# Optimization experiments

Hardware: AMD Instinct MI355X
Metric: run time of the kernel (lower is better)

Reference implementation:

```python
import jax, jax.numpy as jnp
import numpy as np

B, S, H = 64, 2048, 512


def _xavier(key, shape):
    fan_in, fan_out = shape[-1], shape[-2] if len(shape) > 1 else 1
    limit = float(np.sqrt(6.0 / (fan_in + fan_out)))
    return jax.random.uniform(key, shape, jnp.float32, -limit, limit)


def setup_inputs() -> dict:
    key = jax.random.key(0)
    k1, k2, k3, k4, k5, k6 = jax.random.split(key, 6)
    keys_ = jax.random.normal(k1, (B, S, H), jnp.float32)
    query = jax.random.normal(k2, (B, H), jnp.float32)
    v1 = _xavier(k3, (H,))
    W1 = _xavier(k4, (H, 2 * H))
    v2 = _xavier(k5, (H,))
    W2 = _xavier(k6, (H, 2 * H))
    return {"keys": keys_, "query": query, "v1": v1, "W1": W1, "v2": v2, "W2": W2}


def reference(keys, query, v1, W1, v2, W2):
    b, s, h = keys.shape
    # Stage 1: additive (Bahdanau) scoring over concat(keys, broadcast query)
    q = jnp.broadcast_to(query[:, None, :], (b, s, h))          # [B,S,H]
    hidden = jnp.concatenate([keys, q], axis=2)                  # [B,S,2H]
    t1 = jnp.tanh(jnp.einsum('de,bse->bsd', W1, hidden))         # [B,S,H]
    scores = jnp.einsum('d,bsd->bs', v1, t1)                     # [B,S]
    attns = jax.nn.softmax(scores, axis=1)                       # [B,S]
    # values == keys in the original module
    new_q = jnp.einsum('bs,bsh->bh', attns, keys)                # [B,H]
    # Stage 2: score again against concat(keys, broadcast new_query)
    nq = jnp.broadcast_to(new_q[:, None, :], (b, s, h))
    hidden2 = jnp.concatenate([keys, nq], axis=2)                # [B,S,2H]
    t2 = jnp.tanh(jnp.einsum('de,bse->bsd', W2, hidden2))        # [B,S,H]
    attn_vecs = jnp.einsum('d,bsd->bs', v2, t2)[:, None, :]      # [B,1,S]
    return attn_vecs
```

## Files before the change

kernel.cpp:

```cpp
#include <hip/hip_runtime.h>
#include <cstdint>
#include <cstddef>

#define S_DIM 2048

typedef __attribute__((ext_vector_type(8))) short short8;
typedef __attribute__((ext_vector_type(4))) float f32x4;

static __device__ __forceinline__ unsigned short f2bf(float f) {
  union { float f; unsigned int u; } v; v.f = f;
  unsigned int r = (v.u + 0x7fffu + ((v.u >> 16) & 1u)) >> 16;
  return (unsigned short)r;
}

static __device__ __forceinline__ float bf2f(unsigned short u) {
  union { unsigned int u; float f; } v; v.u = ((unsigned int)u) << 16;
  return v.f;
}

static __device__ __forceinline__ float fast_tanh(float x) {
  x = fminf(15.f, fmaxf(-15.f, x));
  float e = __expf(x + x);
  return 1.f - 2.f * __builtin_amdgcn_rcpf(e + 1.f);
}

static __device__ __forceinline__ void gload_lds16(const void* g, void* l) {
  __builtin_amdgcn_global_load_lds(
      (const __attribute__((address_space(1))) void*)g,
      (__attribute__((address_space(3))) void*)l, 16, 0, 0);
}


__global__ __launch_bounds__(256) void pack_b_kernel(
    const float* __restrict__ W1, const float* __restrict__ W2,
    unsigned short* __restrict__ wkp1, unsigned short* __restrict__ wkp2) {
  int j = blockIdx.x * 256 + threadIdx.x;
  const float* W = (j < 32768) ? W1 : W2;
  unsigned short* o = (j < 32768) ? wkp1 : wkp2;
  int wt = j & 32767;
  int k0 = wt >> 11, g = (wt >> 6) & 31, lhi = (wt >> 4) & 3, l15 = wt & 15;
  const float* src = W + (size_t)(g * 16 + l15) * 1024 + k0 * 32 + lhi * 8;
  float4 f0 = *reinterpret_cast<const float4*>(src);
  float4 f1 = *reinterpret_cast<const float4*>(src + 4);
  short8 hv;
  hv[0] = (short)f2bf(f0.x); hv[1] = (short)f2bf(f0.y);
  hv[2] = (short)f2bf(f0.z); hv[3] = (short)f2bf(f0.w);
  hv[4] = (short)f2bf(f1.x); hv[5] = (short)f2bf(f1.y);
  hv[6] = (short)f2bf(f1.z); hv[7] = (short)f2bf(f1.w);
  *reinterpret_cast<short8*>(o + (size_t)wt * 8) = hv;
}

__global__ __launch_bounds__(512, 2) void fused_pack_scores_kernel(
    const float* __restrict__ keys, const unsigned short* __restrict__ wkp,
    const float* __restrict__ v, const float* __restrict__ qp,
    unsigned short* __restrict__ akp, float* __restrict__ scores1) {
  __shared__ __align__(16) unsigned short lds_a[32768];
  __shared__ float lds_score[8][64];

  const int tid  = threadIdx.x;
  const int wid  = tid >> 6;
  const int lane = tid & 63;
  const int l15  = lane & 15;
  const int lhi  = lane >> 4;
  const int tile = blockIdx.x;
  const int row0 = tile * 64;
  const int b    = row0 >> 11;
  const int wcol = wid * 64;

  {
    const int s_mr  = (tid >> 6) & 3;
    const int s_lhi = (tid >> 4) & 3;
    const int s_l15 = tid & 15;
    const int k0_0  = tid >> 8;
    const float* srow =
        keys + (size_t)(row0 + s_mr * 16 + s_l15) * 512 + s_lhi * 8;
    unsigned short* atile = akp + (size_t)tile * 32768;
    float4 f[8][2];
    #pragma unroll
    for (int i = 0; i < 8; ++i) {
      const int k0 = k0_0 + 2 * i;
      const float* src = srow + k0 * 32;
      f[i][0] = *reinterpret_cast<const float4*>(src);
      f[i][1] = *reinterpret_cast<const float4*>(src + 4);
    }
    __builtin_amdgcn_sched_barrier(0);
    #pragma unroll
    for (int i = 0; i < 8; ++i) {
      const int c = i * 512 + tid;
      short8 hv;
      hv[0] = (short)f2bf(f[i][0].x); hv[1] = (short)f2bf(f[i][0].y);
      hv[2] = (short)f2bf(f[i][0].z); hv[3] = (short)f2bf(f[i][0].w);
      hv[4] = (short)f2bf(f[i][1].x); hv[5] = (short)f2bf(f[i][1].y);
      hv[6] = (short)f2bf(f[i][1].z); hv[7] = (short)f2bf(f[i][1].w);
      *reinterpret_cast<short8*>((char*)lds_a + c * 16) = hv;
      *reinterpret_cast<short8*>(atile + (size_t)c * 8) = hv;
    }
  }

  const unsigned short* wbase = wkp + (size_t)wid * 2048 + (size_t)lane * 8;
  short8 bb[2][4];
  #pragma unroll
  for (int nc = 0; nc < 4; ++nc)
    bb[0][nc] = *reinterpret_cast<const short8*>(wbase + nc * 512);

  __syncthreads();

  f32x4 acc[4][4];
  #pragma unroll
  for (int mr = 0; mr < 4; ++mr)
    #pragma unroll
    for (int nc = 0; nc < 4; ++nc) {
      f32x4 z = {0.f, 0.f, 0.f, 0.f};
      acc[mr][nc] = z;
    }

  const char* abase = (const char*)lds_a + lane * 16;

  #pragma unroll
  for (int k0 = 0; k0 < 16; ++k0) {
    const int cur = k0 & 1, nxt = cur ^ 1;
    if (k0 < 15) {
      #pragma unroll
      for (int nc = 0; nc < 4; ++nc)
        bb[nxt][nc] = *reinterpret_cast<const short8*>(
            wbase + (size_t)(k0 + 1) * 16384 + nc * 512);
    }
    short8 a[4];
    #pragma unroll
    for (int mr = 0; mr < 4; ++mr)
      a[mr] = *reinterpret_cast<const short8*>(abase + k0 * 4096 + mr * 1024);
    #pragma unroll
    for (int mr = 0; mr < 4; ++mr)
      #pragma unroll
      for (int nc = 0; nc < 4; ++nc)
        acc[mr][nc] = __builtin_amdgcn_mfma_f32_16x16x32_bf16(
            a[mr], bb[cur][nc], acc[mr][nc], 0, 0, 0);
  }

  float rp[4][4];
  #pragma unroll
  for (int mr = 0; mr < 4; ++mr)
    #pragma unroll
    for (int j = 0; j < 4; ++j) rp[mr][j] = 0.f;

  #pragma unroll
  for (int nc = 0; nc < 4; ++nc) {
    int col = wcol + nc * 16 + l15;
    float vv = v[col];
    float qv = qp[b * 512 + col];
    #pragma unroll
    for (int mr = 0; mr < 4; ++mr)
      #pragma unroll
      for (int j = 0; j < 4; ++j)
        rp[mr][j] += fast_tanh(acc[mr][nc][j] + qv) * vv;
  }

  #pragma unroll
  for (int off = 1; off < 16; off <<= 1)
    #pragma unroll
    for (int mr = 0; mr < 4; ++mr)
      #pragma unroll
      for (int j = 0; j < 4; ++j)
        rp[mr][j] += __shfl_xor(rp[mr][j], off, 64);

  if (l15 == 0) {
    #pragma unroll
    for (int mr = 0; mr < 4; ++mr)
      #pragma unroll
      for (int j = 0; j < 4; ++j)
        lds_score[wid][mr * 16 + lhi * 4 + j] = rp[mr][j];
  }
  __syncthreads();
  if (tid < 64) {
    float s = 0.f;
    #pragma unroll
    for (int w = 0; w < 8; ++w) s += lds_score[w][tid];
    scores1[row0 + tid] = s;
  }
}

__global__ __launch_bounds__(512, 4) void fused_packed_kernel(
    const unsigned short* __restrict__ akp, const unsigned short* __restrict__ wkp,
    const float* __restrict__ v, const float* __restrict__ qp,
    float* __restrict__ out) {
  __shared__ __align__(16) unsigned short lds_a[32768];
  __shared__ float lds_score[8][64];

  const int tid  = threadIdx.x;
  const int wid  = tid >> 6;
  const int lane = tid & 63;
  const int l15  = lane & 15;
  const int lhi  = lane >> 4;
  const int tile = blockIdx.x;
  const int row0 = tile * 64;
  const int b    = row0 >> 11;
  const int wcol = wid * 64;

  const unsigned short* atile = akp + (size_t)tile * 32768;
  #pragma unroll
  for (int i = 0; i < 8; ++i)
    gload_lds16(atile + (i * 512 + tid) * 8, (char*)lds_a + (i * 512 + tid) * 16);

  const unsigned short* wbase = wkp + (size_t)wid * 2048 + (size_t)lane * 8;
  short8 bb[2][4];
  #pragma unroll
  for (int nc = 0; nc < 4; ++nc)
    bb[0][nc] = *reinterpret_cast<const short8*>(wbase + nc * 512);

  __syncthreads();

  f32x4 acc[4][4];
  #pragma unroll
  for (int mr = 0; mr < 4; ++mr)
    #pragma unroll
    for (int nc = 0; nc < 4; ++nc) {
      f32x4 z = {0.f, 0.f, 0.f, 0.f};
      acc[mr][nc] = z;
    }

  const char* abase = (const char*)lds_a + lane * 16;

  #pragma unroll
  for (int k0 = 0; k0 < 16; ++k0) {
    const int cur = k0 & 1, nxt = cur ^ 1;
    if (k0 < 15) {
      #pragma unroll
      for (int nc = 0; nc < 4; ++nc)
        bb[nxt][nc] = *reinterpret_cast<const short8*>(
            wbase + (size_t)(k0 + 1) * 16384 + nc * 512);
    }
    short8 a[4];
    #pragma unroll
    for (int mr = 0; mr < 4; ++mr)
      a[mr] = *reinterpret_cast<const short8*>(abase + k0 * 4096 + mr * 1024);
    #pragma unroll
    for (int mr = 0; mr < 4; ++mr)
      #pragma unroll
      for (int nc = 0; nc < 4; ++nc)
        acc[mr][nc] = __builtin_amdgcn_mfma_f32_16x16x32_bf16(
            a[mr], bb[cur][nc], acc[mr][nc], 0, 0, 0);
  }

  float rp[4][4];
  #pragma unroll
  for (int mr = 0; mr < 4; ++mr)
    #pragma unroll
    for (int j = 0; j < 4; ++j) rp[mr][j] = 0.f;

  #pragma unroll
  for (int nc = 0; nc < 4; ++nc) {
    int col = wcol + nc * 16 + l15;
    float vv = v[col];
    float qv = qp[b * 512 + col];
    #pragma unroll
    for (int mr = 0; mr < 4; ++mr)
      #pragma unroll
      for (int j = 0; j < 4; ++j)
        rp[mr][j] += fast_tanh(acc[mr][nc][j] + qv) * vv;
  }

  #pragma unroll
  for (int off = 1; off < 16; off <<= 1)
    #pragma unroll
    for (int mr = 0; mr < 4; ++mr)
      #pragma unroll
      for (int j = 0; j < 4; ++j)
        rp[mr][j] += __shfl_xor(rp[mr][j], off, 64);

  if (l15 == 0) {
    #pragma unroll
    for (int mr = 0; mr < 4; ++mr)
      #pragma unroll
      for (int j = 0; j < 4; ++j)
        lds_score[wid][mr * 16 + lhi * 4 + j] = rp[mr][j];
  }
  __syncthreads();
  if (tid < 64) {
    float s = 0.f;
    #pragma unroll
    for (int w = 0; w < 8; ++w) s += lds_score[w][tid];
    out[row0 + tid] = s;
  }
}

__global__ __launch_bounds__(256) void wsum_packed_kernel(
    const unsigned short* __restrict__ akp, const float* __restrict__ attn,
    float* __restrict__ new_q) {
  int b = blockIdx.x, k0 = blockIdx.y;
  int t = threadIdx.x;
  int mr = t >> 6, lhi = (t >> 4) & 3, l15 = t & 15;
  const unsigned short* base =
      akp + (size_t)b * 32 * 32768 + (size_t)k0 * 2048 + (size_t)t * 8;
  const float* ab = attn + b * S_DIM + mr * 16 + l15;
  float acc[8];
  #pragma unroll
  for (int e = 0; e < 8; ++e) acc[e] = 0.f;
  #pragma unroll 4
  for (int tile = 0; tile < 32; ++tile) {
    short8 kv = *reinterpret_cast<const short8*>(base + (size_t)tile * 32768);
    float w = ab[tile * 64];
    #pragma unroll
    for (int e = 0; e < 8; ++e)
      acc[e] += w * bf2f((unsigned short)kv[e]);
  }
  __shared__ float red[4][64][8];
  #pragma unroll
  for (int e = 0; e < 8; ++e) red[lhi][mr * 16 + l15][e] = acc[e];
  __syncthreads();
  if (t < 32) {
    int lh = t >> 3, e = t & 7;
    float s = 0.f;
    #pragma unroll 8
    for (int r = 0; r < 64; ++r) s += red[lh][r][e];
    new_q[b * 512 + k0 * 32 + lh * 8 + e] = s;
  }
}


__global__ __launch_bounds__(512) void qproj_kernel(
    const float* __restrict__ W, const float* __restrict__ x,
    float* __restrict__ qp) {
  __shared__ float xs[512];
  int b = blockIdx.x, d = threadIdx.x;
  xs[d] = x[b * 512 + d];
  __syncthreads();
  const float4* wr = (const float4*)(W + (size_t)d * 1024 + 512);
  const float4* xv = (const float4*)xs;
  float acc = 0.f;
  #pragma unroll 8
  for (int h = 0; h < 128; ++h) {
    float4 w4 = wr[h], x4 = xv[h];
    acc += w4.x * x4.x + w4.y * x4.y + w4.z * x4.z + w4.w * x4.w;
  }
  qp[b * 512 + d] = acc;
}

__global__ __launch_bounds__(256) void softmax_kernel(float* __restrict__ sc) {
  int b = blockIdx.x, tid = threadIdx.x;
  float* row = sc + (size_t)b * S_DIM;
  float vv[8];
  float m = -1e30f;
  #pragma unroll
  for (int i = 0; i < 8; ++i) { vv[i] = row[tid + i * 256]; m = fmaxf(m, vv[i]); }
  #pragma unroll
  for (int off = 32; off; off >>= 1) m = fmaxf(m, __shfl_xor(m, off, 64));
  __shared__ float red[4], red2[4];
  int wid = tid >> 6, lane = tid & 63;
  if (lane == 0) red[wid] = m;
  __syncthreads();
  m = fmaxf(fmaxf(red[0], red[1]), fmaxf(red[2], red[3]));
  float s = 0.f;
  #pragma unroll
  for (int i = 0; i < 8; ++i) { vv[i] = __expf(vv[i] - m); s += vv[i]; }
  #pragma unroll
  for (int off = 32; off; off >>= 1) s += __shfl_xor(s, off, 64);
  if (lane == 0) red2[wid] = s;
  __syncthreads();
  s = red2[0] + red2[1] + red2[2] + red2[3];
  float inv = 1.f / s;
  #pragma unroll
  for (int i = 0; i < 8; ++i) row[tid + i * 256] = vv[i] * inv;
}


__global__ __launch_bounds__(256) void convw_kernel(
    const float* __restrict__ W1, const float* __restrict__ W2,
    unsigned short* __restrict__ wk1, unsigned short* __restrict__ wk2) {
  int idx = blockIdx.x * 256 + threadIdx.x;
  const float* W = (idx < 262144) ? W1 : W2;
  unsigned short* o = (idx < 262144) ? wk1 : wk2;
  int j = idx & 262143;
  int d = j >> 9, h = j & 511;
  o[j] = f2bf(W[(size_t)d * 1024 + h]);
}

__global__ __launch_bounds__(512, 4) void fused_scores_kernel(
    const float* __restrict__ keys, const unsigned short* __restrict__ wk,
    const float* __restrict__ v, const float* __restrict__ qp,
    float* __restrict__ out) {
  __shared__ __align__(16) unsigned short lds_k[64 * 512];
  __shared__ float lds_score[8][64];
  char* lds_b = (char*)lds_k;
  const int tid  = threadIdx.x;
  const int wid  = tid >> 6;
  const int lane = tid & 63;
  const int l15  = lane & 15;
  const int lhi  = lane >> 4;
  const int row0 = blockIdx.x * 64;
  const int b    = row0 >> 11;
  const int wcol = wid * 64;
  #pragma unroll
  for (int i = 0; i < 8; ++i) {
    int c = i * 512 + tid;
    int r = c >> 6, k = (c & 63) * 8;
    const float* src = keys + (size_t)(row0 + r) * 512 + k;
    const float4 f0 = *reinterpret_cast<const float4*>(src);
    const float4 f1 = *reinterpret_cast<const float4*>(src + 4);
    short8 hv;
    hv[0] = (short)f2bf(f0.x); hv[1] = (short)f2bf(f0.y);
    hv[2] = (short)f2bf(f0.z); hv[3] = (short)f2bf(f0.w);
    hv[4] = (short)f2bf(f1.x); hv[5] = (short)f2bf(f1.y);
    hv[6] = (short)f2bf(f1.z); hv[7] = (short)f2bf(f1.w);
    int byte = (r * 1024 + k * 2) ^ ((r & 7) << 4);
    *reinterpret_cast<short8*>(lds_b + byte) = hv;
  }
  __syncthreads();
  f32x4 acc[4][4];
  #pragma unroll
  for (int mr = 0; mr < 4; ++mr)
    #pragma unroll
    for (int nc = 0; nc < 4; ++nc) {
      f32x4 z = {0.f, 0.f, 0.f, 0.f};
      acc[mr][nc] = z;
    }
  const int koff = lhi * 8;
  #pragma unroll 1
  for (int k0 = 0; k0 < 512; k0 += 32) {
    short8 a[4], bbv[4];
    #pragma unroll
    for (int nc = 0; nc < 4; ++nc) {
      const unsigned short* p =
          wk + (((size_t)(wcol + nc * 16 + l15)) << 9) + k0 + koff;
      bbv[nc] = *reinterpret_cast<const short8*>(p);
    }
    #pragma unroll
    for (int mr = 0; mr < 4; ++mr) {
      int r = mr * 16 + l15;
      int byte = (r * 1024 + (k0 + koff) * 2) ^ ((r & 7) << 4);
      a[mr] = *reinterpret_cast<const short8*>(lds_b + byte);
    }
    #pragma unroll
    for (int mr = 0; mr < 4; ++mr)
      #pragma unroll
      for (int nc = 0; nc < 4; ++nc)
        acc[mr][nc] = __builtin_amdgcn_mfma_f32_16x16x32_bf16(
            a[mr], bbv[nc], acc[mr][nc], 0, 0, 0);
  }
  float rp[4][4];
  #pragma unroll
  for (int mr = 0; mr < 4; ++mr)
    #pragma unroll
    for (int j = 0; j < 4; ++j) rp[mr][j] = 0.f;
  #pragma unroll
  for (int nc = 0; nc < 4; ++nc) {
    int col = wcol + nc * 16 + l15;
    float vv = v[col];
    float qv = qp[b * 512 + col];
    #pragma unroll
    for (int mr = 0; mr < 4; ++mr)
      #pragma unroll
      for (int j = 0; j < 4; ++j)
        rp[mr][j] += fast_tanh(acc[mr][nc][j] + qv) * vv;
  }
  #pragma unroll
  for (int off = 1; off < 16; off <<= 1)
    #pragma unroll
    for (int mr = 0; mr < 4; ++mr)
      #pragma unroll
      for (int j = 0; j < 4; ++j)
        rp[mr][j] += __shfl_xor(rp[mr][j], off, 64);
  if (l15 == 0) {
    #pragma unroll
    for (int mr = 0; mr < 4; ++mr)
      #pragma unroll
      for (int j = 0; j < 4; ++j)
        lds_score[wid][mr * 16 + lhi * 4 + j] = rp[mr][j];
  }
  __syncthreads();
  if (tid < 64) {
    float s = 0.f;
    #pragma unroll
    for (int w = 0; w < 8; ++w) s += lds_score[w][tid];
    out[row0 + tid] = s;
  }
}

__global__ __launch_bounds__(512) void wsum_part_kernel(
    const float* __restrict__ keys, const float* __restrict__ attn,
    float* __restrict__ part) {
  int b = blockIdx.x, sc = blockIdx.y;
  int tid = threadIdx.x;
  int c4 = tid & 127, rg = tid >> 7;
  const float* kb = keys + ((size_t)(b * S_DIM + sc * 128 + rg * 32)) * 512 + c4 * 4;
  const float* ab = attn + b * S_DIM + sc * 128 + rg * 32;
  float4 acc = {0.f, 0.f, 0.f, 0.f};
  #pragma unroll 8
  for (int i = 0; i < 32; ++i) {
    float w = ab[i];
    float4 kv = *reinterpret_cast<const float4*>(kb + (size_t)i * 512);
    acc.x += w * kv.x; acc.y += w * kv.y; acc.z += w * kv.z; acc.w += w * kv.w;
  }
  __shared__ float4 red[4][128];
  red[rg][c4] = acc;
  __syncthreads();
  if (tid < 128) {
    float4 a0 = red[0][tid], a1 = red[1][tid], a2 = red[2][tid], a3 = red[3][tid];
    float4 s;
    s.x = a0.x + a1.x + a2.x + a3.x;
    s.y = a0.y + a1.y + a2.y + a3.y;
    s.z = a0.z + a1.z + a2.z + a3.z;
    s.w = a0.w + a1.w + a2.w + a3.w;
    *reinterpret_cast<float4*>(part + ((size_t)b * 16 + sc) * 512 + tid * 4) = s;
  }
}

__global__ __launch_bounds__(512) void wsum_final_kernel(
    const float* __restrict__ part, float* __restrict__ new_q) {
  int b = blockIdx.x, h = threadIdx.x;
  float acc = 0.f;
  #pragma unroll
  for (int sc = 0; sc < 16; ++sc) acc += part[((size_t)b * 16 + sc) * 512 + h];
  new_q[b * 512 + h] = acc;
}


extern "C" void kernel_launch(void* const* d_in, const int* in_sizes, int n_in,
                              void* d_out, int out_size, void* d_ws, size_t ws_size,
                              hipStream_t stream) {
  (void)in_sizes; (void)n_in; (void)out_size;
  const float* keys  = (const float*)d_in[0];
  const float* query = (const float*)d_in[1];
  const float* v1    = (const float*)d_in[2];
  const float* W1    = (const float*)d_in[3];
  const float* v2    = (const float*)d_in[4];
  const float* W2    = (const float*)d_in[5];
  float* out = (float*)d_out;
  float* wsf = (float*)d_ws;

  const size_t FAST_NEED = 491520ull * 4ull + 67108864ull * 2ull;
  if (ws_size >= FAST_NEED) {
    float* qp1   = wsf;
    float* attn  = wsf + 32768;
    float* new_q = wsf + 163840;
    float* qp2   = wsf + 196608;
    unsigned short* wkp1 = (unsigned short*)(wsf + 229376);
    unsigned short* wkp2 = wkp1 + 262144;
    unsigned short* akp  = (unsigned short*)(wsf + 491520);

    pack_b_kernel<<<256, 256, 0, stream>>>(W1, W2, wkp1, wkp2);
    qproj_kernel<<<64, 512, 0, stream>>>(W1, query, qp1);
    fused_pack_scores_kernel<<<2048, 512, 0, stream>>>(keys, wkp1, v1, qp1, akp, attn);
    softmax_kernel<<<64, 256, 0, stream>>>(attn);
    wsum_packed_kernel<<<dim3(64, 16), 256, 0, stream>>>(akp, attn, new_q);
    qproj_kernel<<<64, 512, 0, stream>>>(W2, new_q, qp2);
    fused_packed_kernel<<<2048, 512, 0, stream>>>(akp, wkp2, v2, qp2, out);
  } else {
    float* qp1   = wsf;
    float* attn  = wsf + 32768;
    float* new_q = wsf + 163840;
    float* qp2   = wsf + 196608;
    float* part  = wsf + 229376;
    unsigned short* wk1 = (unsigned short*)(wsf + 753664);
    unsigned short* wk2 = wk1 + 262144;

    convw_kernel<<<2048, 256, 0, stream>>>(W1, W2, wk1, wk2);
    qproj_kernel<<<64, 512, 0, stream>>>(W1, query, qp1);
    fused_scores_kernel<<<2048, 512, 0, stream>>>(keys, wk1, v1, qp1, attn);
    softmax_kernel<<<64, 256, 0, stream>>>(attn);
    wsum_part_kernel<<<dim3(64, 16), 512, 0, stream>>>(keys, attn, part);
    wsum_final_kernel<<<64, 512, 0, stream>>>(part, new_q);
    qproj_kernel<<<64, 512, 0, stream>>>(W2, new_q, qp2);
    fused_scores_kernel<<<2048, 512, 0, stream>>>(keys, wk2, v2, qp2, out);
  }
}
```

Baseline: 306.7 us.

## Shrink scoring tiles to 32 rows with 4 waves covering 128 columns each

Both fused scoring kernels now process 32-row tiles with 256-thread blocks instead of 64-row tiles with 512 threads. Each wave computes a 2x8 MFMA block over 128 output columns rather than 4x4 over 64 columns, and the B-fragment double buffering is replaced by loading all 8 fragments per k-step. The packed A-tile layout is kept compatible by addressing half-tiles inside the original 64-row packed blocks. The aim is to raise occupancy through halved LDS per block and to double the block count for better load balance. In exchange, W is reread from global/L2 twice as often per row and the k-loop no longer prefetches B ahead of use.

```diff
diff --git a/kernel.cpp b/kernel.cpp
--- a/kernel.cpp
+++ b/kernel.cpp
@@ -50,12 +50,12 @@
   *reinterpret_cast<short8*>(o + (size_t)wt * 8) = hv;
 }
 
-__global__ __launch_bounds__(512, 2) void fused_pack_scores_kernel(
+__global__ __launch_bounds__(256, 4) void fused_pack_scores32_kernel(
     const float* __restrict__ keys, const unsigned short* __restrict__ wkp,
     const float* __restrict__ v, const float* __restrict__ qp,
     unsigned short* __restrict__ akp, float* __restrict__ scores1) {
-  __shared__ __align__(16) unsigned short lds_a[32768];
-  __shared__ float lds_score[8][64];
+  __shared__ __align__(16) unsigned short lds_a[16384];
+  __shared__ float lds_score[4][32];
 
   const int tid  = threadIdx.x;
   const int wid  = tid >> 6;
@@ -63,128 +63,119 @@
   const int l15  = lane & 15;
   const int lhi  = lane >> 4;
   const int tile = blockIdx.x;
-  const int row0 = tile * 64;
+  const int row0 = tile * 32;
   const int b    = row0 >> 11;
-  const int wcol = wid * 64;
+  const int t64  = tile >> 1;
+  const int half = tile & 1;
 
   {
-    const int s_mr  = (tid >> 6) & 3;
-    const int s_lhi = (tid >> 4) & 3;
-    const int s_l15 = tid & 15;
-    const int k0_0  = tid >> 8;
+    const int m_   = (tid >> 6) & 1;
+    const int lhi_ = (tid >> 4) & 3;
+    const int l15_ = tid & 15;
+    const int k0b  = tid >> 7;
+    const int mrG  = 2 * half + m_;
     const float* srow =
-        keys + (size_t)(row0 + s_mr * 16 + s_l15) * 512 + s_lhi * 8;
-    unsigned short* atile = akp + (size_t)tile * 32768;
-    float4 f[8][2];
-    #pragma unroll
-    for (int i = 0; i < 8; ++i) {
-      const int k0 = k0_0 + 2 * i;
-      const float* src = srow + k0 * 32;
-      f[i][0] = *reinterpret_cast<const float4*>(src);
-      f[i][1] = *reinterpret_cast<const float4*>(src + 4);
-    }
-    __builtin_amdgcn_sched_barrier(0);
-    #pragma unroll
-    for (int i = 0; i < 8; ++i) {
-      const int c = i * 512 + tid;
-      short8 hv;
-      hv[0] = (short)f2bf(f[i][0].x); hv[1] = (short)f2bf(f[i][0].y);
-      hv[2] = (short)f2bf(f[i][0].z); hv[3] = (short)f2bf(f[i][0].w);
-      hv[4] = (short)f2bf(f[i][1].x); hv[5] = (short)f2bf(f[i][1].y);
-      hv[6] = (short)f2bf(f[i][1].z); hv[7] = (short)f2bf(f[i][1].w);
-      *reinterpret_cast<short8*>((char*)lds_a + c * 16) = hv;
-      *reinterpret_cast<short8*>(atile + (size_t)c * 8) = hv;
-    }
-  }
-
-  const unsigned short* wbase = wkp + (size_t)wid * 2048 + (size_t)lane * 8;
-  short8 bb[2][4];
-  #pragma unroll
-  for (int nc = 0; nc < 4; ++nc)
-    bb[0][nc] = *reinterpret_cast<const short8*>(wbase + nc * 512);
-
-  __syncthreads();
-
-  f32x4 acc[4][4];
-  #pragma unroll
-  for (int mr = 0; mr < 4; ++mr)
-    #pragma unroll
-    for (int nc = 0; nc < 4; ++nc) {
+        keys + (size_t)(row0 + m_ * 16 + l15_) * 512 + lhi_ * 8;
+    unsigned short* at = akp + (size_t)t64 * 32768;
+    #pragma unroll
+    for (int g = 0; g < 2; ++g) {
+      float4 f[4][2];
+      #pragma unroll
+      for (int i = 0; i < 4; ++i) {
+        const int k0 = (g * 4 + i) * 2 + k0b;
+        const float* src = srow + k0 * 32;
+        f[i][0] = *reinterpret_cast<const float4*>(src);
+        f[i][1] = *reinterpret_cast<const float4*>(src + 4);
+      }
+      __builtin_amdgcn_sched_barrier(0);
+      #pragma unroll
+      for (int i = 0; i < 4; ++i) {
+        const int k0 = (g * 4 + i) * 2 + k0b;
+        short8 hv;
+        hv[0] = (short)f2bf(f[i][0].x); hv[1] = (short)f2bf(f[i][0].y);
+        hv[2] = (short)f2bf(f[i][0].z); hv[3] = (short)f2bf(f[i][0].w);
+        hv[4] = (short)f2bf(f[i][1].x); hv[5] = (short)f2bf(f[i][1].y);
+        hv[6] = (short)f2bf(f[i][1].z); hv[7] = (short)f2bf(f[i][1].w);
+        const int c = k0 * 128 + m_ * 64 + lhi_ * 16 + l15_;
+        *reinterpret_cast<short8*>((char*)lds_a + c * 16) = hv;
+        *reinterpret_cast<short8*>(
+            at + ((size_t)k0 * 256 + mrG * 64 + lhi_ * 16 + l15_) * 8) = hv;
+      }
+    }
+  }
+  __syncthreads();
+
+  f32x4 acc[2][8];
+  #pragma unroll
+  for (int mr = 0; mr < 2; ++mr)
+    #pragma unroll
+    for (int nc = 0; nc < 8; ++nc) {
       f32x4 z = {0.f, 0.f, 0.f, 0.f};
       acc[mr][nc] = z;
     }
 
+  const unsigned short* wbase =
+      wkp + (size_t)(wid * 8) * 512 + (size_t)lane * 8;
   const char* abase = (const char*)lds_a + lane * 16;
 
   #pragma unroll
   for (int k0 = 0; k0 < 16; ++k0) {
-    const int cur = k0 & 1, nxt = cur ^ 1;
-    if (k0 < 15) {
-      #pragma unroll
-      for (int nc = 0; nc < 4; ++nc)
-        bb[nxt][nc] = *reinterpret_cast<const short8*>(
-            wbase + (size_t)(k0 + 1) * 16384 + nc * 512);
-    }
-    short8 a[4];
-    #pragma unroll
-    for (int mr = 0; mr < 4; ++mr)
-      a[mr] = *reinterpret_cast<const short8*>(abase + k0 * 4096 + mr * 1024);
-    #pragma unroll
-    for (int mr = 0; mr < 4; ++mr)
-      #pragma unroll
-      for (int nc = 0; nc < 4; ++nc)
-        acc[mr][nc] = __builtin_amdgcn_mfma_f32_16x16x32_bf16(
-            a[mr], bb[cur][nc], acc[mr][nc], 0, 0, 0);
-  }
-
-  float rp[4][4];
-  #pragma unroll
-  for (int mr = 0; mr < 4; ++mr)
+    short8 bbv[8];
+    #pragma unroll
+    for (int nc = 0; nc < 8; ++nc)
+      bbv[nc] = *reinterpret_cast<const short8*>(
+          wbase + (size_t)k0 * 16384 + nc * 512);
+    short8 a0 = *reinterpret_cast<const short8*>(abase + k0 * 2048);
+    short8 a1 = *reinterpret_cast<const short8*>(abase + k0 * 2048 + 1024);
+    #pragma unroll
+    for (int nc = 0; nc < 8; ++nc) {
+      acc[0][nc] = __builtin_amdgcn_mfma_f32_16x16x32_bf16(a0, bbv[nc], acc[0][nc], 0, 0, 0);
+      acc[1][nc] = __builtin_amdgcn_mfma_f32_16x16x32_bf16(a1, bbv[nc], acc[1][nc], 0, 0, 0);
+    }
+  }
+
+  float rp[2][4];
+  #pragma unroll
+  for (int mr = 0; mr < 2; ++mr)
     #pragma unroll
     for (int j = 0; j < 4; ++j) rp[mr][j] = 0.f;
-
-  #pragma unroll
-  for (int nc = 0; nc < 4; ++nc) {
-    int col = wcol + nc * 16 + l15;
-    float vv = v[col];
-    float qv = qp[b * 512 + col];
-    #pragma unroll
-    for (int mr = 0; mr < 4; ++mr)
+  #pragma unroll
+  for (int nc = 0; nc < 8; ++nc) {
+    const int col = wid * 128 + nc * 16 + l15;
+    const float vv = v[col];
+    const float qv = qp[b * 512 + col];
+    #pragma unroll
+    for (int mr = 0; mr < 2; ++mr)
       #pragma unroll
       for (int j = 0; j < 4; ++j)
         rp[mr][j] += fast_tanh(acc[mr][nc][j] + qv) * vv;
   }
-
   #pragma unroll
   for (int off = 1; off < 16; off <<= 1)
     #pragma unroll
-    for (int mr = 0; mr < 4; ++mr)
+    for (int mr = 0; mr < 2; ++mr)
       #pragma unroll
       for (int j = 0; j < 4; ++j)
         rp[mr][j] += __shfl_xor(rp[mr][j], off, 64);
-
   if (l15 == 0) {
     #pragma unroll
-    for (int mr = 0; mr < 4; ++mr)
+    for (int mr = 0; mr < 2; ++mr)
       #pragma unroll
       for (int j = 0; j < 4; ++j)
         lds_score[wid][mr * 16 + lhi * 4 + j] = rp[mr][j];
   }
   __syncthreads();
-  if (tid < 64) {
-    float s = 0.f;
-    #pragma unroll
-    for (int w = 0; w < 8; ++w) s += lds_score[w][tid];
-    scores1[row0 + tid] = s;
-  }
-}
-
-__global__ __launch_bounds__(512, 4) void fused_packed_kernel(
+  if (tid < 32)
+    scores1[row0 + tid] = lds_score[0][tid] + lds_score[1][tid] +
+                          lds_score[2][tid] + lds_score[3][tid];
+}
+
+__global__ __launch_bounds__(256, 4) void fused_packed32_kernel(
     const unsigned short* __restrict__ akp, const unsigned short* __restrict__ wkp,
     const float* __restrict__ v, const float* __restrict__ qp,
     float* __restrict__ out) {
-  __shared__ __align__(16) unsigned short lds_a[32768];
-  __shared__ float lds_score[8][64];
+  __shared__ __align__(16) unsigned short lds_a[16384];
+  __shared__ float lds_score[4][32];
 
   const int tid  = threadIdx.x;
   const int wid  = tid >> 6;
@@ -192,95 +183,89 @@
   const int l15  = lane & 15;
   const int lhi  = lane >> 4;
   const int tile = blockIdx.x;
-  const int row0 = tile * 64;
+  const int row0 = tile * 32;
   const int b    = row0 >> 11;
-  const int wcol = wid * 64;
-
-  const unsigned short* atile = akp + (size_t)tile * 32768;
-  #pragma unroll
-  for (int i = 0; i < 8; ++i)
-    gload_lds16(atile + (i * 512 + tid) * 8, (char*)lds_a + (i * 512 + tid) * 16);
-
-  const unsigned short* wbase = wkp + (size_t)wid * 2048 + (size_t)lane * 8;
-  short8 bb[2][4];
-  #pragma unroll
-  for (int nc = 0; nc < 4; ++nc)
-    bb[0][nc] = *reinterpret_cast<const short8*>(wbase + nc * 512);
-
-  __syncthreads();
-
-  f32x4 acc[4][4];
-  #pragma unroll
-  for (int mr = 0; mr < 4; ++mr)
-    #pragma unroll
-    for (int nc = 0; nc < 4; ++nc) {
+  const int t64  = tile >> 1;
+  const int half = tile & 1;
+
+  {
+    const int k0b  = tid >> 7;
+    const int m_   = (tid >> 6) & 1;
+    const int low6 = tid & 63;
+    const int mrG  = 2 * half + m_;
+    const unsigned short* at = akp + (size_t)t64 * 32768;
+    #pragma unroll
+    for (int i = 0; i < 8; ++i) {
+      const int k0 = i * 2 + k0b;
+      gload_lds16(at + ((size_t)k0 * 256 + mrG * 64 + low6) * 8,
+                  (char*)lds_a + (i * 256 + tid) * 16);
+    }
+  }
+  __syncthreads();
+
+  f32x4 acc[2][8];
+  #pragma unroll
+  for (int mr = 0; mr < 2; ++mr)
+    #pragma unroll
+    for (int nc = 0; nc < 8; ++nc) {
       f32x4 z = {0.f, 0.f, 0.f, 0.f};
       acc[mr][nc] = z;
     }
 
+  const unsigned short* wbase =
+      wkp + (size_t)(wid * 8) * 512 + (size_t)lane * 8;
   const char* abase = (const char*)lds_a + lane * 16;
 
   #pragma unroll
   for (int k0 = 0; k0 < 16; ++k0) {
-    const int cur = k0 & 1, nxt = cur ^ 1;
-    if (k0 < 15) {
-      #pragma unroll
-      for (int nc = 0; nc < 4; ++nc)
-        bb[nxt][nc] = *reinterpret_cast<const short8*>(
-            wbase + (size_t)(k0 + 1) * 16384 + nc * 512);
-    }
-    short8 a[4];
-    #pragma unroll
-    for (int mr = 0; mr < 4; ++mr)
-      a[mr] = *reinterpret_cast<const short8*>(abase + k0 * 4096 + mr * 1024);
-    #pragma unroll
-    for (int mr = 0; mr < 4; ++mr)
-      #pragma unroll
-      for (int nc = 0; nc < 4; ++nc)
-        acc[mr][nc] = __builtin_amdgcn_mfma_f32_16x16x32_bf16(
-            a[mr], bb[cur][nc], acc[mr][nc], 0, 0, 0);
-  }
-
-  float rp[4][4];
-  #pragma unroll
-  for (int mr = 0; mr < 4; ++mr)
+    short8 bbv[8];
+    #pragma unroll
+    for (int nc = 0; nc < 8; ++nc)
+      bbv[nc] = *reinterpret_cast<const short8*>(
+          wbase + (size_t)k0 * 16384 + nc * 512);
+    short8 a0 = *reinterpret_cast<const short8*>(abase + k0 * 2048);
+    short8 a1 = *reinterpret_cast<const short8*>(abase + k0 * 2048 + 1024);
+    #pragma unroll
+    for (int nc = 0; nc < 8; ++nc) {
+      acc[0][nc] = __builtin_amdgcn_mfma_f32_16x16x32_bf16(a0, bbv[nc], acc[0][nc], 0, 0, 0);
+      acc[1][nc] = __builtin_amdgcn_mfma_f32_16x16x32_bf16(a1, bbv[nc], acc[1][nc], 0, 0, 0);
+    }
+  }
+
+  float rp[2][4];
+  #pragma unroll
+  for (int mr = 0; mr < 2; ++mr)
     #pragma unroll
     for (int j = 0; j < 4; ++j) rp[mr][j] = 0.f;
-
-  #pragma unroll
-  for (int nc = 0; nc < 4; ++nc) {
-    int col = wcol + nc * 16 + l15;
-    float vv = v[col];
-    float qv = qp[b * 512 + col];
-    #pragma unroll
-    for (int mr = 0; mr < 4; ++mr)
+  #pragma unroll
+  for (int nc = 0; nc < 8; ++nc) {
+    const int col = wid * 128 + nc * 16 + l15;
+    const float vv = v[col];
+    const float qv = qp[b * 512 + col];
+    #pragma unroll
+    for (int mr = 0; mr < 2; ++mr)
       #pragma unroll
       for (int j = 0; j < 4; ++j)
         rp[mr][j] += fast_tanh(acc[mr][nc][j] + qv) * vv;
   }
-
   #pragma unroll
   for (int off = 1; off < 16; off <<= 1)
     #pragma unroll
-    for (int mr = 0; mr < 4; ++mr)
+    for (int mr = 0; mr < 2; ++mr)
       #pragma unroll
       for (int j = 0; j < 4; ++j)
         rp[mr][j] += __shfl_xor(rp[mr][j], off, 64);
-
   if (l15 == 0) {
     #pragma unroll
-    for (int mr = 0; mr < 4; ++mr)
+    for (int mr = 0; mr < 2; ++mr)
       #pragma unroll
       for (int j = 0; j < 4; ++j)
         lds_score[wid][mr * 16 + lhi * 4 + j] = rp[mr][j];
   }
   __syncthreads();
-  if (tid < 64) {
-    float s = 0.f;
-    #pragma unroll
-    for (int w = 0; w < 8; ++w) s += lds_score[w][tid];
-    out[row0 + tid] = s;
-  }
+  if (tid < 32)
+    out[row0 + tid] = lds_score[0][tid] + lds_score[1][tid] +
+                      lds_score[2][tid] + lds_score[3][tid];
 }
 
 __global__ __launch_bounds__(256) void wsum_packed_kernel(
@@ -539,11 +524,12 @@
 
     pack_b_kernel<<<256, 256, 0, stream>>>(W1, W2, wkp1, wkp2);
     qproj_kernel<<<64, 512, 0, stream>>>(W1, query, qp1);
-    fused_pack_scores_kernel<<<2048, 512, 0, stream>>>(keys, wkp1, v1, qp1, akp, attn);
+    fused_pack_scores32_kernel<<<4096, 256, 0, stream>>>(
+        keys, wkp1, v1, qp1, akp, attn);
     softmax_kernel<<<64, 256, 0, stream>>>(attn);
     wsum_packed_kernel<<<dim3(64, 16), 256, 0, stream>>>(akp, attn, new_q);
     qproj_kernel<<<64, 512, 0, stream>>>(W2, new_q, qp2);
-    fused_packed_kernel<<<2048, 512, 0, stream>>>(akp, wkp2, v2, qp2, out);
+    fused_packed32_kernel<<<4096, 256, 0, stream>>>(akp, wkp2, v2, qp2, out);
   } else {
     float* qp1   = wsf;
     float* attn  = wsf + 32768;
```

New measurement: 370.6 us. 20.8% more time.
